# Performance work log

Hardware: AMD Instinct MI355X
Metric: run time of the kernel (lower is better)

The kernel has to match this reference:

```python
import jax, jax.numpy as jnp
import numpy as np

B, N, M, D = 4, 2048, 4096, 1
C, K = 4, 32
POINTS_PER_UNIT = 20


def setup_inputs() -> dict:
    key = jax.random.key(0)
    k1, k2, k3 = jax.random.split(key, 3)
    xz = jax.random.uniform(k1, (M, D), dtype=jnp.float32) * 4.0 - 2.0  # grid locations
    x = jax.random.uniform(k2, (B, N, D), dtype=jnp.float32) * 4.0 - 2.0  # target locations
    z = jax.random.normal(k3, (B, C, M, K), dtype=jnp.float32)
    log_scale = jnp.array([np.log(2.0 / POINTS_PER_UNIT)], dtype=jnp.float32)
    return {"xz": xz, "x": x, "z": z, "log_scale": log_scale}


def reference(xz, x, z, log_scale):
    # pairwise squared distances between grid xz [M,D] and targets x [B,N,D] -> [B,M,N]
    d2 = jnp.sum((xz[None, :, None, :] - x[:, None, :, :]) ** 2, axis=-1)
    # RBF weights (note: divided by exp(log_scale), matching original code)
    w = jnp.exp(-0.5 * d2 / jnp.exp(log_scale[0]))  # [B,M,N]
    # weights^T @ z with channel broadcast: [B,C,N,K]
    zt = jnp.einsum('bmn,bcmk->bcnk', w, z)
    # outer product z @ z^T: [B,C,N,N] positive semi-definite
    out = jnp.einsum('bcnk,bcmk->bcnm', zt, zt)
    return (xz, out)
```

## Files before the change

### kernel.cpp

```cpp
#include <hip/hip_runtime.h>
#include <hip/hip_bf16.h>

#define B_   4
#define N_   2048
#define M_   4096
#define C_   4
#define K_   32
#define CK_  128
#define M32_ 128

typedef float f32x4 __attribute__((ext_vector_type(4)));
typedef short s16x8 __attribute__((ext_vector_type(8)));

__device__ __forceinline__ short f2bf(float f) {
    union { __hip_bfloat16 h; short s; } u;
    u.h = __float2bfloat16(f);
    return u.s;
}
__device__ __forceinline__ float bf2f(unsigned short u) {
    return __uint_as_float((unsigned)u << 16);
}

__global__ __launch_bounds__(256) void z2frag_kernel(
    const float* __restrict__ z, unsigned short* __restrict__ zf,
    const float* __restrict__ xz, float* __restrict__ out)
{
    const unsigned u = blockIdx.x * 256 + threadIdx.x;
    const int s   = u & 63;
    const int lg  = s >> 4, l15 = s & 15;
    const int m32 = (u >> 6) & (M32_ - 1);
    const int g   = (u >> 13) & 7;
    const int b   = u >> 16;
    const int c   = g >> 1;
    const int k   = (g & 1) * 16 + l15;
    const int m0  = m32 * 32 + lg * 8;

    const float* src = &z[(((size_t)(b * C_ + c)) * M_ + m0) * K_ + k];
    s16x8 pk;
    #pragma unroll
    for (int e = 0; e < 8; ++e) pk[e] = f2bf(src[(size_t)e * K_]);
    *(s16x8*)&zf[(size_t)u * 8] = pk;

    if (u < 1024) *(f32x4*)&out[u * 4] = *(const f32x4*)&xz[u * 4];
}

template <int MS>
__global__ __launch_bounds__(512, 4) void zt_mfma_kernel(
    const float* __restrict__ xz, const float* __restrict__ x,
    const unsigned short* __restrict__ zf, const float* __restrict__ ls,
    unsigned short* __restrict__ ztp)
{
    constexpr int MCH = M_ / MS;
    constexpr int L   = MCH / 32;
    __shared__ __align__(16) float xz_s[MCH];

    const int tid  = threadIdx.x;
    const int lane = tid & 63;
    const int w    = tid >> 6;
    const int wq   = w >> 1;
    const int wc   = w & 1;
    const int l15  = lane & 15;
    const int lg   = lane >> 4;
    const int ms   = blockIdx.x;
    const int nblk = blockIdx.y * 128;
    const int b    = blockIdx.z;

    const float coef2 = -0.5f * __expf(-ls[0]) * 1.4426950408889634f;

    float xv[2];
    #pragma unroll
    for (int fa = 0; fa < 2; ++fa)
        xv[fa] = x[b * N_ + nblk + wq * 32 + fa * 16 + l15];

    const int mstart = ms * MCH;
    for (int i = tid; i < MCH; i += 512) xz_s[i] = xz[mstart + i];
    __syncthreads();

    f32x4 acc[2][4];
    #pragma unroll
    for (int i = 0; i < 2; ++i)
        #pragma unroll
        for (int j = 0; j < 4; ++j) acc[i][j] = (f32x4)0.0f;

    const unsigned short* fbase =
        &zf[(((size_t)(b * 8 + wc * 4)) * M32_ + mstart / 32) * 512 + lane * 8];

    s16x8 nb[4];
    #pragma unroll
    for (int fc = 0; fc < 4; ++fc)
        nb[fc] = *(const s16x8*)&fbase[(size_t)fc * M32_ * 512];

    #pragma unroll 4
    for (int ms32 = 0; ms32 < L; ++ms32) {
        s16x8 cb[4];
        #pragma unroll
        for (int fc = 0; fc < 4; ++fc) cb[fc] = nb[fc];
        if (ms32 + 1 < L) {
            #pragma unroll
            for (int fc = 0; fc < 4; ++fc)
                nb[fc] = *(const s16x8*)&fbase[((size_t)fc * M32_ + ms32 + 1) * 512];
        }
        const float* xzp = &xz_s[ms32 * 32 + lg * 8];
        const f32x4 t0 = *reinterpret_cast<const f32x4*>(xzp);
        const f32x4 t1 = *reinterpret_cast<const f32x4*>(xzp + 4);
        const float tt[8] = {t0.x, t0.y, t0.z, t0.w, t1.x, t1.y, t1.z, t1.w};
        s16x8 af[2];
        #pragma unroll
        for (int fa = 0; fa < 2; ++fa) {
            #pragma unroll
            for (int j = 0; j < 8; ++j) {
                const float d = tt[j] - xv[fa];
                af[fa][j] = f2bf(exp2f(coef2 * d * d));
            }
        }
        #pragma unroll
        for (int fa = 0; fa < 2; ++fa)
            #pragma unroll
            for (int fc = 0; fc < 4; ++fc)
                acc[fa][fc] = __builtin_amdgcn_mfma_f32_16x16x32_bf16(
                    af[fa], cb[fc], acc[fa][fc], 0, 0, 0);
    }

    unsigned short* dst = ztp + (size_t)ms * (B_ * C_ * N_ * K_);
    #pragma unroll
    for (int fc = 0; fc < 4; ++fc) {
        const int ck = wc * 64 + fc * 16 + l15;
        const int c  = ck >> 5, k = ck & 31;
        #pragma unroll
        for (int fa = 0; fa < 2; ++fa) {
            const int n0 = nblk + wq * 32 + fa * 16 + lg * 4;
            #pragma unroll
            for (int r = 0; r < 4; ++r)
                dst[(((size_t)b * C_ + c) * N_ + n0 + r) * K_ + k] =
                    (unsigned short)f2bf(acc[fa][fc][r]);
        }
    }
}

template <int MS>
__global__ __launch_bounds__(256) void zt_reduce_kernel(
    const unsigned short* __restrict__ ztp, unsigned short* __restrict__ ztb)
{
    const size_t t      = (size_t)blockIdx.x * 256 + threadIdx.x;
    const size_t stride = (size_t)(B_ * C_ * N_ * K_);
    float s0 = 0.f, s1 = 0.f, s2 = 0.f, s3 = 0.f;
    #pragma unroll
    for (int p = 0; p < MS; ++p) {
        const ushort4 v = *(const ushort4*)&ztp[(size_t)p * stride + t * 4];
        s0 += bf2f(v.x); s1 += bf2f(v.y); s2 += bf2f(v.z); s3 += bf2f(v.w);
    }
    ushort4 pk;
    pk.x = (unsigned short)f2bf(s0); pk.y = (unsigned short)f2bf(s1);
    pk.z = (unsigned short)f2bf(s2); pk.w = (unsigned short)f2bf(s3);
    *(ushort4*)&ztb[t * 4] = pk;
}

__global__ __launch_bounds__(256, 2) void out_mfma_sym_kernel(
    const unsigned short* __restrict__ ztb, float* __restrict__ out)
{
    __shared__ __align__(16) float t_s[64][132];
    __shared__ __align__(16) float t2 [128][68];

    const int tid  = threadIdx.x;
    const int lane = tid & 63;
    const int wave = tid >> 6;
    const int wn   = wave >> 1;
    const int wm   = wave & 1;
    const int l15  = lane & 15;
    const int lg   = lane >> 4;

    const int xid = blockIdx.y;
    int tj = (int)((sqrtf(8.f * xid + 1.f) - 1.f) * 0.5f);
    while (tj * (tj + 1) / 2 > xid) --tj;
    while ((tj + 1) * (tj + 2) / 2 <= xid) ++tj;
    const int ti   = xid - tj * (tj + 1) / 2;
    const int nblk = ti * 128;
    const int mblk = tj * 128;
    const int bc   = blockIdx.x;

    const unsigned short* base = ztb + (size_t)bc * (N_ * K_);

    s16x8 afr[4], bfr[4];
    #pragma unroll
    for (int f = 0; f < 4; ++f) {
        const int n = nblk + wn * 64 + f * 16 + l15;
        afr[f] = *reinterpret_cast<const s16x8*>(&base[(size_t)n * K_ + lg * 8]);
        const int m = mblk + wm * 64 + f * 16 + l15;
        bfr[f] = *reinterpret_cast<const s16x8*>(&base[(size_t)m * K_ + lg * 8]);
    }

    f32x4 acc[4][4];
    #pragma unroll
    for (int i = 0; i < 4; ++i)
        #pragma unroll
        for (int j = 0; j < 4; ++j) acc[i][j] = (f32x4)0.0f;

    #pragma unroll
    for (int fa = 0; fa < 4; ++fa)
        #pragma unroll
        for (int fm = 0; fm < 4; ++fm)
            acc[fa][fm] = __builtin_amdgcn_mfma_f32_16x16x32_bf16(
                afr[fa], bfr[fm], acc[fa][fm], 0, 0, 0);

    float* ob = out + (size_t)bc * N_ * N_;
    const bool offdiag = (ti != tj);

    #pragma unroll
    for (int p = 0; p < 2; ++p) {
        if (p) __syncthreads();
        if (wn == p) {
            #pragma unroll
            for (int fa = 0; fa < 4; ++fa) {
                const int row0 = fa * 16 + lg * 4;
                #pragma unroll
                for (int fm = 0; fm < 4; ++fm) {
                    const int mcol = wm * 64 + fm * 16 + l15;
                    #pragma unroll
                    for (int r = 0; r < 4; ++r)
                        t_s[row0 + r][mcol] = acc[fa][fm][r];
                    *(f32x4*)&t2[mcol][row0] = acc[fa][fm];
                }
            }
        }
        __syncthreads();
        #pragma unroll
        for (int it = 0; it < 8; ++it) {
            const int e   = tid + it * 256;
            const int row = e >> 5;
            const int c4  = e & 31;
            const f32x4 v = *reinterpret_cast<const f32x4*>(&t_s[row][c4 * 4]);
            *(f32x4*)&ob[(size_t)(nblk + p * 64 + row) * N_ + mblk + c4 * 4] = v;
        }
        if (offdiag) {
            #pragma unroll
            for (int it = 0; it < 8; ++it) {
                const int e    = tid + it * 256;
                const int mrow = e >> 4;
                const int nc4  = e & 15;
                const f32x4 v  = *reinterpret_cast<const f32x4*>(&t2[mrow][nc4 * 4]);
                *(f32x4*)&ob[(size_t)(mblk + mrow) * N_ + nblk + p * 64 + nc4 * 4] = v;
            }
        }
    }
}

extern "C" void kernel_launch(void* const* d_in, const int* in_sizes, int n_in,
                              void* d_out, int out_size, void* d_ws, size_t ws_size,
                              hipStream_t stream)
{
    const float* xz = (const float*)d_in[0];
    const float* x  = (const float*)d_in[1];
    const float* z  = (const float*)d_in[2];
    const float* ls = (const float*)d_in[3];
    float* out = (float*)d_out;

    (void)in_sizes; (void)n_in; (void)out_size;

    const size_t ztf = (size_t)B_ * C_ * N_ * K_;
    unsigned short* ztb = (unsigned short*)d_ws;
    unsigned short* zf  = ztb + ztf;
    unsigned short* ztp = zf + (size_t)B_ * CK_ * M_;

    z2frag_kernel<<<dim3((unsigned)(B_ * 8 * M32_ * 64 / 256)), dim3(256), 0, stream>>>(
        z, zf, xz, out);

    const size_t base_b = ztf * 2 + (size_t)B_ * CK_ * M_ * 2;
    if (ws_size >= base_b + (size_t)8 * ztf * 2) {
        zt_mfma_kernel<8><<<dim3(8, N_ / 128, B_), dim3(512), 0, stream>>>(xz, x, zf, ls, ztp);
        zt_reduce_kernel<8><<<dim3(1024), dim3(256), 0, stream>>>(ztp, ztb);
    } else if (ws_size >= base_b + (size_t)4 * ztf * 2) {
        zt_mfma_kernel<4><<<dim3(4, N_ / 128, B_), dim3(512), 0, stream>>>(xz, x, zf, ls, ztp);
        zt_reduce_kernel<4><<<dim3(1024), dim3(256), 0, stream>>>(ztp, ztb);
    } else {
        zt_mfma_kernel<2><<<dim3(2, N_ / 128, B_), dim3(512), 0, stream>>>(xz, x, zf, ls, ztp);
        zt_reduce_kernel<2><<<dim3(1024), dim3(256), 0, stream>>>(ztp, ztb);
    }

    out_mfma_sym_kernel<<<dim3(B_ * C_, 136), dim3(256), 0, stream>>>(ztb, out + M_);
}
```

Measured before the change: 87.87 us.

## Drop split-M partial sums and reduce kernel; split zt over N and channel halves

The zt GEMM no longer splits the M reduction across blocks and writes partial bf16 results, so the separate reduce kernel and its workspace traffic go away. Each block now covers 64 targets and half of the C*K columns over the full M range, with a two-deep prefetch of z fragments. The out kernel grid is transposed so the tile index varies fastest. In exchange, each wave loops over all of M with fewer MFMAs per exp computation, so the RBF weights are recomputed for each column half. This may shift the zt stage toward exp/VALU work and lengthen its serial loop.

```diff
diff --git a/kernel.cpp b/kernel.cpp
--- a/kernel.cpp
+++ b/kernel.cpp
@@ -16,9 +16,6 @@
     union { __hip_bfloat16 h; short s; } u;
     u.h = __float2bfloat16(f);
     return u.s;
-}
-__device__ __forceinline__ float bf2f(unsigned short u) {
-    return __uint_as_float((unsigned)u << 16);
 }
 
 __global__ __launch_bounds__(256) void z2frag_kernel(
@@ -44,15 +41,12 @@
     if (u < 1024) *(f32x4*)&out[u * 4] = *(const f32x4*)&xz[u * 4];
 }
 
-template <int MS>
 __global__ __launch_bounds__(512, 4) void zt_mfma_kernel(
     const float* __restrict__ xz, const float* __restrict__ x,
     const unsigned short* __restrict__ zf, const float* __restrict__ ls,
-    unsigned short* __restrict__ ztp)
-{
-    constexpr int MCH = M_ / MS;
-    constexpr int L   = MCH / 32;
-    __shared__ __align__(16) float xz_s[MCH];
+    unsigned short* __restrict__ ztb)
+{
+    __shared__ __align__(16) float xz_s[M_];
 
     const int tid  = threadIdx.x;
     const int lane = tid & 63;
@@ -61,98 +55,65 @@
     const int wc   = w & 1;
     const int l15  = lane & 15;
     const int lg   = lane >> 4;
-    const int ms   = blockIdx.x;
-    const int nblk = blockIdx.y * 128;
+    const int nblk = blockIdx.x * 64;
+    const int ckh  = blockIdx.y;
     const int b    = blockIdx.z;
 
     const float coef2 = -0.5f * __expf(-ls[0]) * 1.4426950408889634f;
 
-    float xv[2];
-    #pragma unroll
-    for (int fa = 0; fa < 2; ++fa)
-        xv[fa] = x[b * N_ + nblk + wq * 32 + fa * 16 + l15];
-
-    const int mstart = ms * MCH;
-    for (int i = tid; i < MCH; i += 512) xz_s[i] = xz[mstart + i];
+    const float xv = x[b * N_ + nblk + wq * 16 + l15];
+
+    for (int i = tid; i < M_; i += 512) xz_s[i] = xz[i];
     __syncthreads();
 
-    f32x4 acc[2][4];
-    #pragma unroll
-    for (int i = 0; i < 2; ++i)
-        #pragma unroll
-        for (int j = 0; j < 4; ++j) acc[i][j] = (f32x4)0.0f;
+    f32x4 acc[2];
+    acc[0] = (f32x4)0.0f; acc[1] = (f32x4)0.0f;
 
     const unsigned short* fbase =
-        &zf[(((size_t)(b * 8 + wc * 4)) * M32_ + mstart / 32) * 512 + lane * 8];
-
-    s16x8 nb[4];
-    #pragma unroll
-    for (int fc = 0; fc < 4; ++fc)
-        nb[fc] = *(const s16x8*)&fbase[(size_t)fc * M32_ * 512];
+        &zf[((size_t)(b * 8 + ckh * 4 + wc * 2)) * M32_ * 512 + lane * 8];
+
+    s16x8 p0[2], p1[2];
+    #pragma unroll
+    for (int fc = 0; fc < 2; ++fc) {
+        p0[fc] = *(const s16x8*)&fbase[(size_t)fc * M32_ * 512];
+        p1[fc] = *(const s16x8*)&fbase[((size_t)fc * M32_ + 1) * 512];
+    }
 
     #pragma unroll 4
-    for (int ms32 = 0; ms32 < L; ++ms32) {
-        s16x8 cb[4];
-        #pragma unroll
-        for (int fc = 0; fc < 4; ++fc) cb[fc] = nb[fc];
-        if (ms32 + 1 < L) {
+    for (int ms32 = 0; ms32 < M32_; ++ms32) {
+        s16x8 cb[2];
+        cb[0] = p0[0]; cb[1] = p0[1];
+        p0[0] = p1[0]; p0[1] = p1[1];
+        if (ms32 + 2 < M32_) {
             #pragma unroll
-            for (int fc = 0; fc < 4; ++fc)
-                nb[fc] = *(const s16x8*)&fbase[((size_t)fc * M32_ + ms32 + 1) * 512];
+            for (int fc = 0; fc < 2; ++fc)
+                p1[fc] = *(const s16x8*)&fbase[((size_t)fc * M32_ + ms32 + 2) * 512];
         }
         const float* xzp = &xz_s[ms32 * 32 + lg * 8];
         const f32x4 t0 = *reinterpret_cast<const f32x4*>(xzp);
         const f32x4 t1 = *reinterpret_cast<const f32x4*>(xzp + 4);
         const float tt[8] = {t0.x, t0.y, t0.z, t0.w, t1.x, t1.y, t1.z, t1.w};
-        s16x8 af[2];
-        #pragma unroll
-        for (int fa = 0; fa < 2; ++fa) {
-            #pragma unroll
-            for (int j = 0; j < 8; ++j) {
-                const float d = tt[j] - xv[fa];
-                af[fa][j] = f2bf(exp2f(coef2 * d * d));
-            }
-        }
-        #pragma unroll
-        for (int fa = 0; fa < 2; ++fa)
-            #pragma unroll
-            for (int fc = 0; fc < 4; ++fc)
-                acc[fa][fc] = __builtin_amdgcn_mfma_f32_16x16x32_bf16(
-                    af[fa], cb[fc], acc[fa][fc], 0, 0, 0);
-    }
-
-    unsigned short* dst = ztp + (size_t)ms * (B_ * C_ * N_ * K_);
-    #pragma unroll
-    for (int fc = 0; fc < 4; ++fc) {
-        const int ck = wc * 64 + fc * 16 + l15;
+        s16x8 af;
+        #pragma unroll
+        for (int j = 0; j < 8; ++j) {
+            const float d = tt[j] - xv;
+            af[j] = f2bf(exp2f(coef2 * d * d));
+        }
+        #pragma unroll
+        for (int fc = 0; fc < 2; ++fc)
+            acc[fc] = __builtin_amdgcn_mfma_f32_16x16x32_bf16(af, cb[fc], acc[fc], 0, 0, 0);
+    }
+
+    #pragma unroll
+    for (int fc = 0; fc < 2; ++fc) {
+        const int ck = ckh * 64 + wc * 32 + fc * 16 + l15;
         const int c  = ck >> 5, k = ck & 31;
-        #pragma unroll
-        for (int fa = 0; fa < 2; ++fa) {
-            const int n0 = nblk + wq * 32 + fa * 16 + lg * 4;
-            #pragma unroll
-            for (int r = 0; r < 4; ++r)
-                dst[(((size_t)b * C_ + c) * N_ + n0 + r) * K_ + k] =
-                    (unsigned short)f2bf(acc[fa][fc][r]);
-        }
-    }
-}
-
-template <int MS>
-__global__ __launch_bounds__(256) void zt_reduce_kernel(
-    const unsigned short* __restrict__ ztp, unsigned short* __restrict__ ztb)
-{
-    const size_t t      = (size_t)blockIdx.x * 256 + threadIdx.x;
-    const size_t stride = (size_t)(B_ * C_ * N_ * K_);
-    float s0 = 0.f, s1 = 0.f, s2 = 0.f, s3 = 0.f;
-    #pragma unroll
-    for (int p = 0; p < MS; ++p) {
-        const ushort4 v = *(const ushort4*)&ztp[(size_t)p * stride + t * 4];
-        s0 += bf2f(v.x); s1 += bf2f(v.y); s2 += bf2f(v.z); s3 += bf2f(v.w);
-    }
-    ushort4 pk;
-    pk.x = (unsigned short)f2bf(s0); pk.y = (unsigned short)f2bf(s1);
-    pk.z = (unsigned short)f2bf(s2); pk.w = (unsigned short)f2bf(s3);
-    *(ushort4*)&ztb[t * 4] = pk;
+        const int n0 = nblk + wq * 16 + lg * 4;
+        #pragma unroll
+        for (int r = 0; r < 4; ++r)
+            ztb[(((size_t)b * C_ + c) * N_ + n0 + r) * K_ + k] =
+                (unsigned short)f2bf(acc[fc][r]);
+    }
 }
 
 __global__ __launch_bounds__(256, 2) void out_mfma_sym_kernel(
@@ -169,14 +130,14 @@
     const int l15  = lane & 15;
     const int lg   = lane >> 4;
 
-    const int xid = blockIdx.y;
+    const int xid = blockIdx.x;
     int tj = (int)((sqrtf(8.f * xid + 1.f) - 1.f) * 0.5f);
     while (tj * (tj + 1) / 2 > xid) --tj;
     while ((tj + 1) * (tj + 2) / 2 <= xid) ++tj;
     const int ti   = xid - tj * (tj + 1) / 2;
     const int nblk = ti * 128;
     const int mblk = tj * 128;
-    const int bc   = blockIdx.x;
+    const int bc   = blockIdx.y;
 
     const unsigned short* base = ztb + (size_t)bc * (N_ * K_);
 
@@ -254,27 +215,16 @@
     const float* ls = (const float*)d_in[3];
     float* out = (float*)d_out;
 
-    (void)in_sizes; (void)n_in; (void)out_size;
+    (void)in_sizes; (void)n_in; (void)out_size; (void)ws_size;
 
     const size_t ztf = (size_t)B_ * C_ * N_ * K_;
     unsigned short* ztb = (unsigned short*)d_ws;
     unsigned short* zf  = ztb + ztf;
-    unsigned short* ztp = zf + (size_t)B_ * CK_ * M_;
 
     z2frag_kernel<<<dim3((unsigned)(B_ * 8 * M32_ * 64 / 256)), dim3(256), 0, stream>>>(
         z, zf, xz, out);
 
-    const size_t base_b = ztf * 2 + (size_t)B_ * CK_ * M_ * 2;
-    if (ws_size >= base_b + (size_t)8 * ztf * 2) {
-        zt_mfma_kernel<8><<<dim3(8, N_ / 128, B_), dim3(512), 0, stream>>>(xz, x, zf, ls, ztp);
-        zt_reduce_kernel<8><<<dim3(1024), dim3(256), 0, stream>>>(ztp, ztb);
-    } else if (ws_size >= base_b + (size_t)4 * ztf * 2) {
-        zt_mfma_kernel<4><<<dim3(4, N_ / 128, B_), dim3(512), 0, stream>>>(xz, x, zf, ls, ztp);
-        zt_reduce_kernel<4><<<dim3(1024), dim3(256), 0, stream>>>(ztp, ztb);
-    } else {
-        zt_mfma_kernel<2><<<dim3(2, N_ / 128, B_), dim3(512), 0, stream>>>(xz, x, zf, ls, ztp);
-        zt_reduce_kernel<2><<<dim3(1024), dim3(256), 0, stream>>>(ztp, ztb);
-    }
-
-    out_mfma_sym_kernel<<<dim3(B_ * C_, 136), dim3(256), 0, stream>>>(ztb, out + M_);
-}
+    zt_mfma_kernel<<<dim3(N_ / 64, 2, B_), dim3(512), 0, stream>>>(xz, x, zf, ls, ztb);
+
+    out_mfma_sym_kernel<<<dim3(136, B_ * C_), dim3(256), 0, stream>>>(ztb, out + M_);
+}
```

Result: slower. 102.9 us (+17.1%).
